# Kernel tuning notes

Hardware: AMD Instinct MI355X
Metric: run time of the kernel (lower is better)

Reference implementation:

```python
import jax, jax.numpy as jnp
import numpy as np

INPUT_SIZE = 512
OUTPUT_SIZE = 512
BATCH = 65536
HIDDEN = [256, 128, 64, 32]


def _linear_params(key, fan_in, fan_out):
    # torch nn.Linear default init: U(-1/sqrt(fan_in), 1/sqrt(fan_in))
    kw, kb = jax.random.split(key)
    bound = 1.0 / np.sqrt(fan_in)
    w = jax.random.uniform(kw, (fan_out, fan_in), jnp.float32, -bound, bound)
    b = jax.random.uniform(kb, (fan_out,), jnp.float32, -bound, bound)
    return w, b


def setup_inputs() -> dict:
    key = jax.random.key(0)
    ks = jax.random.split(key, 6)
    x = jax.random.normal(ks[0], (BATCH, INPUT_SIZE), jnp.float32)
    dims = [INPUT_SIZE] + HIDDEN + [OUTPUT_SIZE]
    inp = {"x": x}
    for i in range(5):
        w, b = _linear_params(ks[i + 1], dims[i], dims[i + 1])
        inp[f"w{i+1}"] = w
        inp[f"b{i+1}"] = b
    return inp


def reference(x, w1, b1, w2, b2, w3, b3, w4, b4, w5, b5):
    sig = jax.nn.sigmoid
    # in_size = number of nonzero entries in row 0 (replaces per-element python loop)
    in_size = jnp.count_nonzero(x[0])  # traced int scalar
    h = sig(x @ w1.T + b1)
    h = sig(h @ w2.T + b2)
    h = sig(h @ w3.T + b3)
    h = sig(h @ w4.T + b4)
    y = h @ w5.T + b5  # [B, OUTPUT_SIZE]
    # out has shape [B, INPUT_SIZE]; out[:, :in_size] = y[:, :in_size]
    # (INPUT_SIZE == OUTPUT_SIZE here, so a prefix mask suffices)
    mask = jnp.arange(INPUT_SIZE) < in_size  # [INPUT_SIZE]
    out = jnp.where(mask[None, :], y, jnp.zeros((), y.dtype))
    return out
```

## Files before the change

### kernel.cpp

```cpp
#include <hip/hip_runtime.h>
#include <hip/hip_bf16.h>
#include <stdint.h>

typedef __attribute__((ext_vector_type(4))) float f32x4;
typedef __attribute__((ext_vector_type(4))) unsigned int u32x4;
typedef __attribute__((ext_vector_type(8))) short short8;

#define MFMA16(a, b, c) __builtin_amdgcn_mfma_f32_16x16x32_bf16((a), (b), (c), 0, 0, 0)

__device__ __forceinline__ uint16_t f2bf(float f) {
  __hip_bfloat16 h = __float2bfloat16(f);
  return __builtin_bit_cast(uint16_t, h);
}

__device__ __forceinline__ float fast_sigmoid(float v) {
  return __builtin_amdgcn_rcpf(1.f + __expf(-v));
}

__device__ __forceinline__ short8 cvt8(f32x4 a, f32x4 b) {
  short8 r;
  r[0] = (short)f2bf(a[0]); r[1] = (short)f2bf(a[1]);
  r[2] = (short)f2bf(a[2]); r[3] = (short)f2bf(a[3]);
  r[4] = (short)f2bf(b[0]); r[5] = (short)f2bf(b[1]);
  r[6] = (short)f2bf(b[2]); r[7] = (short)f2bf(b[3]);
  return r;
}

template <int RB>
__device__ __forceinline__ int swzoff(int row, int bcol) {
  constexpr int SLM = (((RB / 16) < 8 ? (RB / 16) : 8)) - 1;
  return row * RB + (bcol ^ ((row & SLM) << 4));
}

template <int RB>
__device__ __forceinline__ short8 lds_a(const uint16_t* buf, int row0, int k0, int lane) {
  int r = row0 + (lane & 15);
  int bcol = (k0 + ((lane >> 4) << 3)) * 2;
  u32x4 raw = *(const u32x4*)((const char*)buf + swzoff<RB>(r, bcol));
  return __builtin_bit_cast(short8, raw);
}

__device__ __forceinline__ short8 load_frag_f32(const float* M, int ld, int r0, int k0, int lane) {
  const float* p = M + (size_t)(r0 + (lane & 15)) * ld + (k0 + ((lane >> 4) << 3));
  f32x4 a = *(const f32x4*)p;
  f32x4 b = *(const f32x4*)(p + 4);
  return cvt8(a, b);
}

__device__ __forceinline__ short8 load_b_pk(const char* base, int f, int lane) {
  u32x4 raw = *(const u32x4*)(base + (((size_t)f * 64 + lane) << 4));
  return __builtin_bit_cast(short8, raw);
}

template <bool P>
__device__ __forceinline__ short8 bfrag(const char* wp, const float* W, int K,
                                        int f0, int ntg, int KT, int kt, int lane) {
  if constexpr (P) {
    return load_b_pk(wp, f0 + ntg * KT + kt, lane);
  } else {
    return load_frag_f32(W, K, ntg * 16, kt * 32, lane);
  }
}

__global__ void pack_kernel(const float* __restrict__ w1, const float* __restrict__ w2,
                            const float* __restrict__ w3, const float* __restrict__ w4,
                            const float* __restrict__ w5, char* __restrict__ ws) {
  int b = blockIdx.x, lane = threadIdx.x;
  const float* W;
  int K, f0;
  if (b < 256)      { W = w1; K = 512; f0 = 0; }
  else if (b < 320) { W = w2; K = 256; f0 = 256; }
  else if (b < 336) { W = w3; K = 128; f0 = 320; }
  else if (b < 340) { W = w4; K = 64;  f0 = 336; }
  else              { W = w5; K = 32;  f0 = 340; }
  int f = b - f0;
  int KT = K / 32;
  int nt = f / KT, kt = f % KT;
  short8 r = load_frag_f32(W, K, nt * 16, kt * 32, lane);
  *(u32x4*)(ws + (((size_t)b * 64 + lane) << 4)) = __builtin_bit_cast(u32x4, r);
}

__device__ __forceinline__ void glds_chunk(const float* xbase, char* sring, int c,
                                           int wid, int lane) {
  char* sb = sring + (size_t)(c & 3) * 8192;
#pragma unroll
  for (int i = 0; i < 2; ++i) {
    int p = wid * 128 + i * 64 + lane;
    int r = p >> 3;
    int q = (p & 7) ^ (r & 7);
    const float* src = xbase + (size_t)r * 512 + c * 32 + q * 4;
    __builtin_amdgcn_global_load_lds(
        (const __attribute__((address_space(1))) unsigned int*)src,
        (__attribute__((address_space(3))) unsigned int*)(sb + ((size_t)(wid * 128 + i * 64) << 4)),
        16, 0, 0);
  }
}

__device__ __forceinline__ short8 lds_a_f32(const char* sb, int row0, int lane) {
  int r = row0 + (lane & 15);
  int g = (lane >> 4) << 1;
  int sw = r & 7;
  const char* rowp = sb + (size_t)r * 128;
  f32x4 a = *(const f32x4*)(rowp + ((g ^ sw) << 4));
  f32x4 b = *(const f32x4*)(rowp + (((g + 1) ^ sw) << 4));
  return cvt8(a, b);
}

#define WAITBAR(VN)                                          \
  asm volatile("s_waitcnt vmcnt(" #VN ")" ::: "memory");     \
  __builtin_amdgcn_s_barrier();

#define KSTEP(C, VN)                                                          \
  {                                                                           \
    WAITBAR(VN);                                                              \
    if ((C) < 15) {                                                           \
      _Pragma("unroll") for (int nt = 0; nt < 4; ++nt)                        \
          bfr[((C) + 1) & 1][nt] =                                            \
              bfrag<P>(wp, w1, 512, 0, wid * 4 + nt, 16, (C) + 1, lane);      \
    }                                                                         \
    __builtin_amdgcn_sched_barrier(0);                                        \
    if ((C) < 13) glds_chunk(xbase, smem, (C) + 3, wid, lane);                \
    char* sc = smem + (size_t)((C) & 3) * 8192;                               \
    _Pragma("unroll") for (int m = 0; m < 4; ++m) {                           \
      short8 a = lds_a_f32(sc, m * 16, lane);                                 \
      _Pragma("unroll") for (int nt = 0; nt < 4; ++nt)                        \
          acc[m][nt] = MFMA16(a, bfr[(C) & 1][nt], acc[m][nt]);               \
    }                                                                         \
  }

template <bool P>
__global__ __launch_bounds__(256, 3) void mlp5_kernel(
    const float* __restrict__ x,
    const float* __restrict__ w1, const float* __restrict__ b1,
    const float* __restrict__ w2, const float* __restrict__ b2,
    const float* __restrict__ w3, const float* __restrict__ b3,
    const float* __restrict__ w4, const float* __restrict__ b4,
    const float* __restrict__ w5, const float* __restrict__ b5,
    const char* __restrict__ wp, float* __restrict__ out) {
  __shared__ __align__(16) char smem[32 * 1024];
  uint16_t* H1 = (uint16_t*)smem;
  uint16_t* H2 = (uint16_t*)smem;
  uint16_t* H3 = (uint16_t*)(smem + 16 * 1024);
  uint16_t* H4 = (uint16_t*)(smem + 24 * 1024);

  const int tid = threadIdx.x;
  const int lane = tid & 63;
  const int wid = tid >> 6;
  const int row0 = blockIdx.x * 64;
  const int lr = (lane >> 4) << 2;
  const int lc = lane & 15;

  int in_size = 0;
#pragma unroll
  for (int j = 0; j < 8; ++j) {
    float v = x[j * 64 + lane];
    in_size += (int)__popcll(__ballot(v != 0.f));
  }

  const float* xbase = x + (size_t)row0 * 512;

  f32x4 acc[4][4];
#pragma unroll
  for (int m = 0; m < 4; ++m)
#pragma unroll
    for (int n = 0; n < 4; ++n) acc[m][n] = (f32x4){0.f, 0.f, 0.f, 0.f};

  short8 bfr[2][4];
  glds_chunk(xbase, smem, 0, wid, lane);
#pragma unroll
  for (int nt = 0; nt < 4; ++nt)
    bfr[0][nt] = bfrag<P>(wp, w1, 512, 0, wid * 4 + nt, 16, 0, lane);
  glds_chunk(xbase, smem, 1, wid, lane);
  glds_chunk(xbase, smem, 2, wid, lane);

  KSTEP(0, 4)  KSTEP(1, 2)  KSTEP(2, 2)  KSTEP(3, 2)
  KSTEP(4, 2)  KSTEP(5, 2)  KSTEP(6, 2)  KSTEP(7, 2)
  KSTEP(8, 2)  KSTEP(9, 2)  KSTEP(10, 2) KSTEP(11, 2)
  KSTEP(12, 2) KSTEP(13, 2) KSTEP(14, 0) KSTEP(15, 0)

  short8 bfr2[2][8];
#pragma unroll
  for (int n = 0; n < 2; ++n)
#pragma unroll
    for (int kt = 0; kt < 8; ++kt)
      bfr2[n][kt] = bfrag<P>(wp, w2, 256, 256, wid * 2 + n, 8, kt, lane);

  __syncthreads();

#pragma unroll
  for (int n = 0; n < 4; ++n) {
    const int ncol = wid * 64 + n * 16;
    const float bv = b1[ncol + lc];
#pragma unroll
    for (int m = 0; m < 4; ++m)
#pragma unroll
      for (int i = 0; i < 4; ++i) {
        float v = fast_sigmoid(acc[m][n][i] + bv);
        *(uint16_t*)((char*)H1 + swzoff<512>(m * 16 + lr + i, (ncol + lc) * 2)) = f2bf(v);
      }
  }
  __syncthreads();

  {
    f32x4 acc2[4][2];
#pragma unroll
    for (int m = 0; m < 4; ++m)
#pragma unroll
      for (int n = 0; n < 2; ++n) acc2[m][n] = (f32x4){0.f, 0.f, 0.f, 0.f};
#pragma unroll
    for (int m = 0; m < 4; ++m) {
#pragma unroll
      for (int kt = 0; kt < 8; ++kt) {
        short8 afr = lds_a<512>(H1, m * 16, kt * 32, lane);
        acc2[m][0] = MFMA16(afr, bfr2[0][kt], acc2[m][0]);
        acc2[m][1] = MFMA16(afr, bfr2[1][kt], acc2[m][1]);
      }
    }
    short8 bfr3[4];
#pragma unroll
    for (int kt = 0; kt < 4; ++kt)
      bfr3[kt] = bfrag<P>(wp, w3, 128, 320, wid, 4, kt, lane);
    __syncthreads();
#pragma unroll
    for (int n = 0; n < 2; ++n) {
      const int ncol = wid * 32 + n * 16;
      const float bv = b2[ncol + lc];
#pragma unroll
      for (int m = 0; m < 4; ++m)
#pragma unroll
        for (int i = 0; i < 4; ++i) {
          float v = fast_sigmoid(acc2[m][n][i] + bv);
          *(uint16_t*)((char*)H2 + swzoff<256>(m * 16 + lr + i, (ncol + lc) * 2)) = f2bf(v);
        }
    }
    __syncthreads();

    f32x4 acc3[4];
#pragma unroll
    for (int m = 0; m < 4; ++m) acc3[m] = (f32x4){0.f, 0.f, 0.f, 0.f};
#pragma unroll
    for (int m = 0; m < 4; ++m)
#pragma unroll
      for (int kt = 0; kt < 4; ++kt) {
        short8 afr = lds_a<256>(H2, m * 16, kt * 32, lane);
        acc3[m] = MFMA16(afr, bfr3[kt], acc3[m]);
      }
    short8 bfr4[2];
#pragma unroll
    for (int kt = 0; kt < 2; ++kt)
      bfr4[kt] = bfrag<P>(wp, w4, 64, 336, wid & 1, 2, kt, lane);
    {
      const int ncol = wid * 16;
      const float bv = b3[ncol + lc];
#pragma unroll
      for (int m = 0; m < 4; ++m)
#pragma unroll
        for (int i = 0; i < 4; ++i) {
          float v = fast_sigmoid(acc3[m][i] + bv);
          *(uint16_t*)((char*)H3 + swzoff<128>(m * 16 + lr + i, (ncol + lc) * 2)) = f2bf(v);
        }
    }
    __syncthreads();

    const int wm = wid >> 1, wn = wid & 1;
    f32x4 acc4[2];
#pragma unroll
    for (int mt = 0; mt < 2; ++mt) acc4[mt] = (f32x4){0.f, 0.f, 0.f, 0.f};
#pragma unroll
    for (int mt = 0; mt < 2; ++mt)
#pragma unroll
      for (int kt = 0; kt < 2; ++kt) {
        short8 afr = lds_a<128>(H3, wm * 32 + mt * 16, kt * 32, lane);
        acc4[mt] = MFMA16(afr, bfr4[kt], acc4[mt]);
      }
    short8 bfr5[8];
#pragma unroll
    for (int nt = 0; nt < 8; ++nt)
      bfr5[nt] = bfrag<P>(wp, w5, 32, 340, wid * 8 + nt, 1, 0, lane);
    {
      const int ncol = wn * 16;
      const float bv = b4[ncol + lc];
#pragma unroll
      for (int mt = 0; mt < 2; ++mt)
#pragma unroll
        for (int i = 0; i < 4; ++i) {
          float v = fast_sigmoid(acc4[mt][i] + bv);
          *(uint16_t*)((char*)H4 + swzoff<64>(wm * 32 + mt * 16 + lr + i, (ncol + lc) * 2)) = f2bf(v);
        }
    }
    __syncthreads();

#pragma unroll
    for (int m = 0; m < 4; ++m) {
      short8 afr = lds_a<64>(H4, m * 16, 0, lane);
#pragma unroll
      for (int nt = 0; nt < 8; ++nt) {
        f32x4 av = MFMA16(afr, bfr5[nt], ((f32x4){0.f, 0.f, 0.f, 0.f}));
        const int col = wid * 128 + nt * 16 + lc;
        const float bv = b5[col];
        const bool keep = col < in_size;
#pragma unroll
        for (int i = 0; i < 4; ++i) {
          float v = keep ? (av[i] + bv) : 0.f;
          out[(size_t)(row0 + m * 16 + lr + i) * 512 + col] = v;
        }
      }
    }
  }
}

extern "C" void kernel_launch(void* const* d_in, const int* in_sizes, int n_in,
                              void* d_out, int out_size, void* d_ws, size_t ws_size,
                              hipStream_t stream) {
  const float* x  = (const float*)d_in[0];
  const float* w1 = (const float*)d_in[1];
  const float* b1 = (const float*)d_in[2];
  const float* w2 = (const float*)d_in[3];
  const float* b2 = (const float*)d_in[4];
  const float* w3 = (const float*)d_in[5];
  const float* b3 = (const float*)d_in[6];
  const float* w4 = (const float*)d_in[7];
  const float* b4 = (const float*)d_in[8];
  const float* w5 = (const float*)d_in[9];
  const float* b5 = (const float*)d_in[10];
  float* out = (float*)d_out;

  dim3 grid(65536 / 64);
  dim3 block(256);
  const bool packed = ws_size >= (size_t)(372 * 1024);
  if (packed) {
    pack_kernel<<<372, 64, 0, stream>>>(w1, w2, w3, w4, w5, (char*)d_ws);
    mlp5_kernel<true><<<grid, block, 0, stream>>>(x, w1, b1, w2, b2, w3, b3, w4, b4,
                                                  w5, b5, (const char*)d_ws, out);
  } else {
    mlp5_kernel<false><<<grid, block, 0, stream>>>(x, w1, b1, w2, b2, w3, b3, w4, b4,
                                                   w5, b5, nullptr, out);
  }
}
```

Baseline: 76.91 us.

## Stage layer-1 input through registers as bf16 into padded LDS double buffer

Replaces the 4-deep asynchronous global-to-LDS fp32 ring for the first layer's input with a register prefetch two chunks ahead. Each chunk is converted to bf16 in registers and written into a 2-slot LDS buffer with an 80-byte padded row stride. This halves LDS footprint and read traffic and does the fp32-to-bf16 conversion once per element instead of in every MFMA fragment read. The trade-off is that global load latency is now hidden by only about one k-step of MFMA work, where the old async ring kept three chunks in flight.

Result: slower. 78.66 us (+2.3%).

```diff
diff --git a/kernel.cpp b/kernel.cpp
--- a/kernel.cpp
+++ b/kernel.cpp
@@ -38,6 +38,11 @@
   int bcol = (k0 + ((lane >> 4) << 3)) * 2;
   u32x4 raw = *(const u32x4*)((const char*)buf + swzoff<RB>(r, bcol));
   return __builtin_bit_cast(short8, raw);
+}
+
+__device__ __forceinline__ short8 lds_a_s(const char* sb, int row0, int lane) {
+  int r = row0 + (lane & 15);
+  return *(const short8*)(sb + r * 80 + ((lane >> 4) << 4));
 }
 
 __device__ __forceinline__ short8 load_frag_f32(const float* M, int ld, int r0, int k0, int lane) {
@@ -80,49 +85,32 @@
   *(u32x4*)(ws + (((size_t)b * 64 + lane) << 4)) = __builtin_bit_cast(u32x4, r);
 }
 
-__device__ __forceinline__ void glds_chunk(const float* xbase, char* sring, int c,
-                                           int wid, int lane) {
-  char* sb = sring + (size_t)(c & 3) * 8192;
-#pragma unroll
-  for (int i = 0; i < 2; ++i) {
-    int p = wid * 128 + i * 64 + lane;
-    int r = p >> 3;
-    int q = (p & 7) ^ (r & 7);
-    const float* src = xbase + (size_t)r * 512 + c * 32 + q * 4;
-    __builtin_amdgcn_global_load_lds(
-        (const __attribute__((address_space(1))) unsigned int*)src,
-        (__attribute__((address_space(3))) unsigned int*)(sb + ((size_t)(wid * 128 + i * 64) << 4)),
-        16, 0, 0);
-  }
-}
-
-__device__ __forceinline__ short8 lds_a_f32(const char* sb, int row0, int lane) {
-  int r = row0 + (lane & 15);
-  int g = (lane >> 4) << 1;
-  int sw = r & 7;
-  const char* rowp = sb + (size_t)r * 128;
-  f32x4 a = *(const f32x4*)(rowp + ((g ^ sw) << 4));
-  f32x4 b = *(const f32x4*)(rowp + (((g + 1) ^ sw) << 4));
-  return cvt8(a, b);
-}
-
-#define WAITBAR(VN)                                          \
-  asm volatile("s_waitcnt vmcnt(" #VN ")" ::: "memory");     \
-  __builtin_amdgcn_s_barrier();
-
-#define KSTEP(C, VN)                                                          \
+#define CHUNK_BAR()                                           \
+  asm volatile("s_waitcnt lgkmcnt(0)" ::: "memory");          \
+  __builtin_amdgcn_s_barrier();                               \
+  __builtin_amdgcn_sched_barrier(0);
+
+#define KSTEP(C)                                                              \
   {                                                                           \
-    WAITBAR(VN);                                                              \
-    if ((C) < 15) {                                                           \
+    CHUNK_BAR();                                                              \
+    if ((C) + 2 < 16) {                                                       \
+      const float* p = xrow + ((C) + 2) * 32;                                 \
+      rA[(C) & 1][0] = *(const f32x4*)p;                                      \
+      rA[(C) & 1][1] = *(const f32x4*)(p + 4);                                \
+    }                                                                         \
+    if ((C) + 1 < 16) {                                                       \
       _Pragma("unroll") for (int nt = 0; nt < 4; ++nt)                        \
           bfr[((C) + 1) & 1][nt] =                                            \
               bfrag<P>(wp, w1, 512, 0, wid * 4 + nt, 16, (C) + 1, lane);      \
     }                                                                         \
     __builtin_amdgcn_sched_barrier(0);                                        \
-    if ((C) < 13) glds_chunk(xbase, smem, (C) + 3, wid, lane);                \
-    char* sc = smem + (size_t)((C) & 3) * 8192;                               \
+    if ((C) + 1 < 16) {                                                       \
+      short8 wv = cvt8(rA[((C) + 1) & 1][0], rA[((C) + 1) & 1][1]);           \
+      *(short8*)(sring + (((C) + 1) & 1) * 5120 + swb) = wv;                  \
+    }                                                                         \
+    const char* sc = sring + ((C) & 1) * 5120;                                \
     _Pragma("unroll") for (int m = 0; m < 4; ++m) {                           \
-      short8 a = lds_a_f32(sc, m * 16, lane);                                 \
+      short8 a = lds_a_s(sc, m * 16, lane);                                   \
       _Pragma("unroll") for (int nt = 0; nt < 4; ++nt)                        \
           acc[m][nt] = MFMA16(a, bfr[(C) & 1][nt], acc[m][nt]);               \
     }                                                                         \
@@ -157,7 +145,10 @@
     in_size += (int)__popcll(__ballot(v != 0.f));
   }
 
-  const float* xbase = x + (size_t)row0 * 512;
+  char* sring = smem;
+  const float* xrow =
+      x + (size_t)(row0 + wid * 16 + (lane & 15)) * 512 + ((lane >> 4) << 3);
+  const int swb = (wid * 16 + (lane & 15)) * 80 + ((lane >> 4) << 4);
 
   f32x4 acc[4][4];
 #pragma unroll
@@ -165,18 +156,24 @@
 #pragma unroll
     for (int n = 0; n < 4; ++n) acc[m][n] = (f32x4){0.f, 0.f, 0.f, 0.f};
 
+  f32x4 rA[2][2];
   short8 bfr[2][4];
-  glds_chunk(xbase, smem, 0, wid, lane);
+  rA[0][0] = *(const f32x4*)(xrow + 0);
+  rA[0][1] = *(const f32x4*)(xrow + 4);
+  rA[1][0] = *(const f32x4*)(xrow + 32);
+  rA[1][1] = *(const f32x4*)(xrow + 36);
 #pragma unroll
   for (int nt = 0; nt < 4; ++nt)
     bfr[0][nt] = bfrag<P>(wp, w1, 512, 0, wid * 4 + nt, 16, 0, lane);
-  glds_chunk(xbase, smem, 1, wid, lane);
-  glds_chunk(xbase, smem, 2, wid, lane);
-
-  KSTEP(0, 4)  KSTEP(1, 2)  KSTEP(2, 2)  KSTEP(3, 2)
-  KSTEP(4, 2)  KSTEP(5, 2)  KSTEP(6, 2)  KSTEP(7, 2)
-  KSTEP(8, 2)  KSTEP(9, 2)  KSTEP(10, 2) KSTEP(11, 2)
-  KSTEP(12, 2) KSTEP(13, 2) KSTEP(14, 0) KSTEP(15, 0)
+  {
+    short8 wv = cvt8(rA[0][0], rA[0][1]);
+    *(short8*)(sring + swb) = wv;
+  }
+
+  KSTEP(0)  KSTEP(1)  KSTEP(2)  KSTEP(3)
+  KSTEP(4)  KSTEP(5)  KSTEP(6)  KSTEP(7)
+  KSTEP(8)  KSTEP(9)  KSTEP(10) KSTEP(11)
+  KSTEP(12) KSTEP(13) KSTEP(14) KSTEP(15)
 
   short8 bfr2[2][8];
 #pragma unroll
```
